# Optimization experiments

Measured on AMD Instinct MI355X. Metric: run time of the kernel, lower is better.

The kernel has to match this reference:

```python
import jax, jax.numpy as jnp
import numpy as np

N_NODES = 4096
N_EDGES = 128
D_X = 128
PE_DIM = 64
NUM_WALKS = 10
WALK_LEN = 5
EMBED_ROWS = 10000
EDGE_P = 0.02
NEG_INF = -1e30


def setup_inputs() -> dict:
    key = jax.random.key(0)
    kx, kh, ke = jax.random.split(key, 3)
    x = jax.random.normal(kx, (N_NODES, D_X), dtype=jnp.float32)
    # binary hypergraph incidence matrix (float, as used by torch H @ H.T)
    incidence = (jax.random.uniform(kh, (N_NODES, N_EDGES)) < EDGE_P).astype(jnp.float32)
    embed_weight = jax.random.normal(ke, (EMBED_ROWS, PE_DIM), dtype=jnp.float32) * 0.02
    return {"x": x, "incidence": incidence, "embed_weight": embed_weight}


def _sample_walks(neighbors, num_walks, walk_length, key):
    """Vectorized random walks: [W, L] node ids and [W, L] validity mask.

    Matches the torch loop: uniform multinomial over (H@H.T>0) neighbors with
    the self-loop zeroed, terminating early when a node has no neighbors.
    """
    N = neighbors.shape[0]
    nb = jax.lax.stop_gradient(neighbors) * (1.0 - jnp.eye(N, dtype=neighbors.dtype))
    logits = jnp.where(nb > 0, 0.0, NEG_INF)  # uniform over neighbors
    row_has = nb.sum(axis=1) > 0              # probs.sum() == 0 -> break
    starts = jnp.repeat(jnp.arange(N), num_walks)  # [W]
    W = starts.shape[0]

    def step(carry, k):
        cur, alive = carry
        alive = alive & row_has[cur]
        nxt = jax.random.categorical(k, logits[cur])  # [W]
        nxt = jnp.where(alive, nxt, cur)
        return (nxt, alive), (nxt, alive)

    keys = jax.random.split(key, walk_length - 1)
    _, (steps, valid) = jax.lax.scan(step, (starts, jnp.ones((W,), bool)), keys)
    walk_nodes = jnp.concatenate([starts[None, :], steps], axis=0).T     # [W, L]
    valid = jnp.concatenate([jnp.ones((1, W), bool), valid], axis=0).T   # [W, L]
    return walk_nodes, valid


def reference(x, incidence, embed_weight):
    N = x.shape[0]
    # node_neighbors = (H @ H.T > 0).float()
    neighbors = ((incidence @ incidence.T) > 0).astype(x.dtype)  # [N, N]
    walk_nodes, valid = _sample_walks(neighbors, NUM_WALKS, WALK_LEN, jax.random.key(42))

    # mean embedding of each walk over its valid (actual) length
    lens = valid.sum(axis=1).astype(x.dtype)                 # [W], >= 1
    emb = embed_weight[walk_nodes]                           # [W, L, D]
    m = (emb * valid[..., None]).sum(axis=1) / lens[:, None]  # [W, D]

    # every (walk, position) occurrence contributes m_walk to pe[node]
    idx = jnp.where(valid, walk_nodes, 0).reshape(-1)                      # [W*L]
    contrib = jnp.where(valid[..., None], m[:, None, :], 0.0)
    contrib = contrib.reshape(-1, m.shape[-1])                             # [W*L, D]
    w = valid.astype(x.dtype).reshape(-1)
    pe_sum = jax.ops.segment_sum(contrib, idx, num_segments=N)             # [N, D]
    cnt = jax.ops.segment_sum(w, idx, num_segments=N)                      # [N]
    pe = jnp.where(cnt[:, None] > 0, pe_sum / jnp.maximum(cnt, 1.0)[:, None], 0.0)
    return jnp.concatenate([x, pe], axis=-1)
```

## Files before the change

### kernel.cpp

```cpp
#include <hip/hip_runtime.h>
#include <hip/hip_fp16.h>
#include <stdint.h>

#define N_NODES   4096
#define N_EDGES   128
#define D_X       128
#define PE_DIM    64
#define NUM_WALKS 10
#define WALK_LEN  5
#define N_WALKS_TOT (N_NODES * NUM_WALKS)
#define OUT_COLS  (D_X + PE_DIM)
#define ROW_CAP   512u
#define VCAP      512u

#define OFF_MASKS   0u
#define OFF_DEG     (OFF_MASKS + N_NODES * 16u)
#define OFF_ADJ     (OFF_DEG + N_NODES * 4u)
#define OFF_WM      (OFF_ADJ + N_NODES * ROW_CAP * 2u)
#define OFF_VCNT    (OFF_WM + N_WALKS_TOT * PE_DIM * 2u)
#define OFF_VLIST   (OFF_VCNT + N_NODES * 4u)

__device__ __forceinline__ void tf2x32(uint32_t kk0, uint32_t kk1,
                                       uint32_t x0, uint32_t x1,
                                       uint32_t& o0, uint32_t& o1) {
  const uint32_t kk2 = kk0 ^ kk1 ^ 0x1BD11BDAu;
  x0 += kk0; x1 += kk1;
  auto rnd = [&](int r) {
    x0 += x1;
    x1 = (x1 << r) | (x1 >> (32 - r));
    x1 ^= x0;
  };
  rnd(13); rnd(15); rnd(26); rnd(6);   x0 += kk1; x1 += kk2 + 1u;
  rnd(17); rnd(29); rnd(16); rnd(24);  x0 += kk2; x1 += kk0 + 2u;
  rnd(13); rnd(15); rnd(26); rnd(6);   x0 += kk0; x1 += kk1 + 3u;
  rnd(17); rnd(29); rnd(16); rnd(24);  x0 += kk1; x1 += kk2 + 4u;
  rnd(13); rnd(15); rnd(26); rnd(6);   x0 += kk2; x1 += kk0 + 5u;
  o0 = x0; o1 = x1;
}

__global__ void k_masks(const float* __restrict__ inc,
                        ulonglong2* __restrict__ masks,
                        unsigned int* __restrict__ vcnt) {
  const int wid = threadIdx.x >> 6, lane = threadIdx.x & 63;
  const int i = blockIdx.x * 4 + wid;
  const float a = inc[i * N_EDGES + lane];
  const float b = inc[i * N_EDGES + 64 + lane];
  const unsigned long long m0 = __ballot(a != 0.f);
  const unsigned long long m1 = __ballot(b != 0.f);
  if (lane == 0) {
    masks[i] = make_ulonglong2(m0, m1);
    vcnt[i] = 0u;
  }
}

__global__ void __launch_bounds__(512)
k_adj(const ulonglong2* __restrict__ masks,
      unsigned short* __restrict__ adj, unsigned int* __restrict__ deg) {
  __shared__ ulonglong2 sm[N_NODES];
  for (int k = threadIdx.x; k < N_NODES; k += 512) sm[k] = masks[k];
  __syncthreads();
  const int wid = threadIdx.x >> 6, lane = threadIdx.x & 63;
  const int i = blockIdx.x * 8 + wid;
  const ulonglong2 mi = sm[i];
  unsigned short* row = adj + (unsigned int)i * ROW_CAP;
  unsigned int base = 0;
  for (int g = 0; g < N_NODES / 64; ++g) {
    const int j = g * 64 + lane;
    const ulonglong2 mj = sm[j];
    const bool pred = (((mi.x & mj.x) | (mi.y & mj.y)) != 0ull) && (j != i);
    const unsigned long long bal = __ballot(pred);
    if (pred) {
      const unsigned int off =
          (unsigned int)__popcll(bal & ((1ull << lane) - 1ull));
      const unsigned int pos = base + off;
      if (pos < ROW_CAP) row[pos] = (unsigned short)j;
    }
    base += (unsigned int)__popcll(bal);
  }
  if (lane == 0) deg[i] = (base < ROW_CAP) ? base : ROW_CAP;
}

__global__ void __launch_bounds__(256)
k_walk(const unsigned int* __restrict__ deg,
       const unsigned short* __restrict__ adj,
       const float* __restrict__ embed,
       __half* __restrict__ walk_m,
       unsigned int* __restrict__ vcnt, unsigned short* __restrict__ vlist) {
  const int wid = threadIdx.x >> 6, lane = threadIdx.x & 63;
  const int w = blockIdx.x * 4 + wid;

  uint32_t a0, a1;
  tf2x32(0u, 42u, (uint32_t)w, (uint32_t)(lane & 1), a0, a1);
  const uint32_t rnd0 = __shfl(a0, 0);
  const uint32_t rnd1 = __shfl(a1, 0);
  const uint32_t rnd2 = __shfl(a0, 1);
  const uint32_t rnd3 = __shfl(a1, 1);

  const uint32_t n0 = (uint32_t)w / NUM_WALKS;
  uint32_t n1, n2, n3, n4, nvalid;
  const unsigned int d0 = deg[n0];
  if (d0 == 0) {
    n1 = n2 = n3 = n4 = n0;
    nvalid = 1u;
  } else {
    uint32_t cur = n0;
    unsigned int d;
    cur = adj[(cur << 9) + (uint32_t)(((uint64_t)rnd0 * d0) >> 32)]; n1 = cur;
    d = deg[cur];
    cur = adj[(cur << 9) + (uint32_t)(((uint64_t)rnd1 * d) >> 32)]; n2 = cur;
    d = deg[cur];
    cur = adj[(cur << 9) + (uint32_t)(((uint64_t)rnd2 * d) >> 32)]; n3 = cur;
    d = deg[cur];
    cur = adj[(cur << 9) + (uint32_t)(((uint64_t)rnd3 * d) >> 32)]; n4 = cur;
    nvalid = 5u;
  }

  float s = embed[n0 * PE_DIM + lane];
  if (nvalid == 5u) {
    s += embed[n1 * PE_DIM + lane];
    s += embed[n2 * PE_DIM + lane];
    s += embed[n3 * PE_DIM + lane];
    s += embed[n4 * PE_DIM + lane];
  }
  const float m = s / (float)nvalid;

  walk_m[(unsigned int)w * PE_DIM + lane] = __float2half(m);

  if ((unsigned int)lane < nvalid) {
    uint32_t node = n0;
    if (lane == 1) node = n1;
    if (lane == 2) node = n2;
    if (lane == 3) node = n3;
    if (lane == 4) node = n4;
    const unsigned int slot = atomicAdd(&vcnt[node], 1u);
    if (slot < VCAP) vlist[node * VCAP + slot] = (unsigned short)w;
  }
}

__global__ void __launch_bounds__(256)
k_gather(const __half* __restrict__ walk_m,
         const unsigned int* __restrict__ vcnt,
         const unsigned short* __restrict__ vlist,
         const float* __restrict__ x,
         float* __restrict__ out) {
  const int wid = threadIdx.x >> 6, lane = threadIdx.x & 63;
  const int v = blockIdx.x * 4 + wid;

  const float2 xv = ((const float2*)(x + (unsigned int)v * D_X))[lane];
  ((float2*)(out + (unsigned int)v * OUT_COLS))[lane] = xv;

  unsigned int c = vcnt[v];
  if (c > VCAP) c = VCAP;
  const unsigned short* vl = vlist + (unsigned int)v * VCAP;
  float s = 0.f;
  unsigned int i = 0;
  for (; i + 4 <= c; i += 4) {
    const uint64_t q = *(const uint64_t*)(vl + i);
    const uint32_t w0 = (uint32_t)(q & 0xFFFFull);
    const uint32_t w1 = (uint32_t)((q >> 16) & 0xFFFFull);
    const uint32_t w2 = (uint32_t)((q >> 32) & 0xFFFFull);
    const uint32_t w3 = (uint32_t)(q >> 48);
    const float m0 = __half2float(walk_m[w0 * PE_DIM + lane]);
    const float m1 = __half2float(walk_m[w1 * PE_DIM + lane]);
    const float m2 = __half2float(walk_m[w2 * PE_DIM + lane]);
    const float m3 = __half2float(walk_m[w3 * PE_DIM + lane]);
    s += (m0 + m1) + (m2 + m3);
  }
  for (; i < c; ++i) {
    const uint32_t ww = vl[i];
    s += __half2float(walk_m[ww * PE_DIM + lane]);
  }
  out[(unsigned int)v * OUT_COLS + D_X + lane] = c ? s / (float)c : 0.f;
}

extern "C" void kernel_launch(void* const* d_in, const int* in_sizes, int n_in,
                              void* d_out, int out_size, void* d_ws, size_t ws_size,
                              hipStream_t stream) {
  const float* x   = (const float*)d_in[0];
  const float* inc = (const float*)d_in[1];
  const float* emb = (const float*)d_in[2];
  float* out = (float*)d_out;

  char* ws = (char*)d_ws;
  ulonglong2*     masks = (ulonglong2*)(ws + OFF_MASKS);
  unsigned int*   deg   = (unsigned int*)(ws + OFF_DEG);
  unsigned short* adj   = (unsigned short*)(ws + OFF_ADJ);
  __half*         wm    = (__half*)(ws + OFF_WM);
  unsigned int*   vcnt  = (unsigned int*)(ws + OFF_VCNT);
  unsigned short* vlist = (unsigned short*)(ws + OFF_VLIST);

  k_masks <<<N_NODES / 4, 256, 0, stream>>>(inc, masks, vcnt);
  k_adj   <<<N_NODES / 8, 512, 0, stream>>>(masks, adj, deg);
  k_walk  <<<N_WALKS_TOT / 4, 256, 0, stream>>>(deg, adj, emb, wm, vcnt, vlist);
  k_gather<<<N_NODES / 4, 256, 0, stream>>>(wm, vcnt, vlist, x, out);
}
```

Baseline: 74.24 us.

## Split per-node gather across four waves with shared-memory reduction

k_gather now assigns one node per 256-thread block instead of one node per wave. Each of the four waves accumulates a strided subset of the node's walk list in chunks of eight, and the partial sums are combined through shared memory. The aim is more parallelism and memory-level concurrency in the latency-bound gather over about 50 entries per node. In exchange it launches four times as many blocks, adds a __syncthreads, and has wasted lanes when a node's walk count is small.

```diff
diff --git a/kernel.cpp b/kernel.cpp
--- a/kernel.cpp
+++ b/kernel.cpp
@@ -143,34 +143,36 @@
          const unsigned short* __restrict__ vlist,
          const float* __restrict__ x,
          float* __restrict__ out) {
+  __shared__ float red[4][PE_DIM];
   const int wid = threadIdx.x >> 6, lane = threadIdx.x & 63;
-  const int v = blockIdx.x * 4 + wid;
+  const int v = blockIdx.x;
 
-  const float2 xv = ((const float2*)(x + (unsigned int)v * D_X))[lane];
-  ((float2*)(out + (unsigned int)v * OUT_COLS))[lane] = xv;
+  if (wid == 1) {
+    const float2 xv = ((const float2*)(x + (unsigned int)v * D_X))[lane];
+    ((float2*)(out + (unsigned int)v * OUT_COLS))[lane] = xv;
+  }
 
   unsigned int c = vcnt[v];
   if (c > VCAP) c = VCAP;
   const unsigned short* vl = vlist + (unsigned int)v * VCAP;
+
   float s = 0.f;
-  unsigned int i = 0;
-  for (; i + 4 <= c; i += 4) {
-    const uint64_t q = *(const uint64_t*)(vl + i);
-    const uint32_t w0 = (uint32_t)(q & 0xFFFFull);
-    const uint32_t w1 = (uint32_t)((q >> 16) & 0xFFFFull);
-    const uint32_t w2 = (uint32_t)((q >> 32) & 0xFFFFull);
-    const uint32_t w3 = (uint32_t)(q >> 48);
-    const float m0 = __half2float(walk_m[w0 * PE_DIM + lane]);
-    const float m1 = __half2float(walk_m[w1 * PE_DIM + lane]);
-    const float m2 = __half2float(walk_m[w2 * PE_DIM + lane]);
-    const float m3 = __half2float(walk_m[w3 * PE_DIM + lane]);
-    s += (m0 + m1) + (m2 + m3);
+  for (unsigned int base = (unsigned int)wid * 8u; base < c; base += 32u) {
+#pragma unroll
+    for (int q = 0; q < 8; ++q) {
+      const unsigned int idx = base + (unsigned int)q;
+      const bool ok = idx < c;
+      const unsigned int ww = ok ? (unsigned int)vl[idx] : (unsigned int)vl[0];
+      const float val = __half2float(walk_m[ww * PE_DIM + lane]);
+      s += ok ? val : 0.f;
+    }
   }
-  for (; i < c; ++i) {
-    const uint32_t ww = vl[i];
-    s += __half2float(walk_m[ww * PE_DIM + lane]);
+  red[wid][lane] = s;
+  __syncthreads();
+  if (wid == 0) {
+    const float t = red[0][lane] + red[1][lane] + red[2][lane] + red[3][lane];
+    out[(unsigned int)v * OUT_COLS + D_X + lane] = c ? t / (float)c : 0.f;
   }
-  out[(unsigned int)v * OUT_COLS + D_X + lane] = c ? s / (float)c : 0.f;
 }
 
 extern "C" void kernel_launch(void* const* d_in, const int* in_sizes, int n_in,
@@ -192,5 +194,5 @@
   k_masks <<<N_NODES / 4, 256, 0, stream>>>(inc, masks, vcnt);
   k_adj   <<<N_NODES / 8, 512, 0, stream>>>(masks, adj, deg);
   k_walk  <<<N_WALKS_TOT / 4, 256, 0, stream>>>(deg, adj, emb, wm, vcnt, vlist);
-  k_gather<<<N_NODES / 4, 256, 0, stream>>>(wm, vcnt, vlist, x, out);
+  k_gather<<<N_NODES, 256, 0, stream>>>(wm, vcnt, vlist, x, out);
 }
```

Result: faster. 62.29 us (-16.1%).
